# Optimization experiments

Hardware: AMD Instinct MI355X
Metric: run time of the kernel (lower is better)

Reference implementation:

```python
import jax, jax.numpy as jnp
import numpy as np

NUM_HEADS = 8
NUM_KV_HEADS = 2
HEAD_DIM = 256
HIDDEN = 2048
ROPE_THETA = 10000.0
QUERY_PRE_ATTN_SCALAR = 256.0
SOFTCAP = 50.0


def setup_inputs() -> dict:
    key = jax.random.key(0)
    k1, k2, k3, k4, k5 = jax.random.split(key, 5)
    B, S = 2, 2048
    s = 0.02
    return {
        "hidden_states": jax.random.normal(k1, (B, S, HIDDEN), dtype=jnp.float32),
        "Wq": jax.random.normal(k2, (NUM_HEADS * HEAD_DIM, HIDDEN), dtype=jnp.float32) * s,
        "Wk": jax.random.normal(k3, (NUM_KV_HEADS * HEAD_DIM, HIDDEN), dtype=jnp.float32) * s,
        "Wv": jax.random.normal(k4, (NUM_KV_HEADS * HEAD_DIM, HIDDEN), dtype=jnp.float32) * s,
        "Wo": jax.random.normal(k5, (HIDDEN, NUM_HEADS * HEAD_DIM), dtype=jnp.float32) * s,
    }


def _rope_cos_sin(S, dtype):
    # LlamaRotaryEmbedding: inv_freq over even dims, emb = cat(freqs, freqs)
    inv_freq = 1.0 / (ROPE_THETA ** (jnp.arange(0, HEAD_DIM, 2, dtype=jnp.float32) / HEAD_DIM))
    pos = jnp.arange(S, dtype=jnp.float32)
    freqs = pos[:, None] * inv_freq[None, :]          # [S, D/2]
    emb = jnp.concatenate([freqs, freqs], axis=-1)     # [S, D]
    return jnp.cos(emb).astype(dtype), jnp.sin(emb).astype(dtype)


def _rotate_half(x):
    x1, x2 = x[..., : HEAD_DIM // 2], x[..., HEAD_DIM // 2 :]
    return jnp.concatenate([-x2, x1], axis=-1)


def reference(hidden_states, Wq, Wk, Wv, Wo):
    B, S, _ = hidden_states.shape
    q = jnp.einsum('bsh,dh->bsd', hidden_states, Wq).reshape(B, S, NUM_HEADS, HEAD_DIM).transpose(0, 2, 1, 3)
    k = jnp.einsum('bsh,dh->bsd', hidden_states, Wk).reshape(B, S, NUM_KV_HEADS, HEAD_DIM).transpose(0, 2, 1, 3)
    v = jnp.einsum('bsh,dh->bsd', hidden_states, Wv).reshape(B, S, NUM_KV_HEADS, HEAD_DIM).transpose(0, 2, 1, 3)

    cos, sin = _rope_cos_sin(S, hidden_states.dtype)   # [S, D]
    cos = cos[None, None]                               # [1,1,S,D]
    sin = sin[None, None]
    q = q * cos + _rotate_half(q) * sin
    k = k * cos + _rotate_half(k) * sin

    # GQA expansion: repeat kv heads to match query heads
    groups = NUM_HEADS // NUM_KV_HEADS
    k = jnp.repeat(k, groups, axis=1)                   # [B,H,S,D]
    v = jnp.repeat(v, groups, axis=1)

    scale = QUERY_PRE_ATTN_SCALAR ** -0.5
    scores = jnp.einsum('bhqd,bhkd->bhqk', q, k) * scale
    scores = jnp.tanh(scores / SOFTCAP) * SOFTCAP       # logit softcapping
    probs = jax.nn.softmax(scores, axis=-1)             # NOTE: no causal mask in source
    attn = jnp.einsum('bhqk,bhkd->bhqd', probs, v)
    attn = attn.transpose(0, 2, 1, 3).reshape(B, S, NUM_HEADS * HEAD_DIM)
    return jnp.einsum('bsd,hd->bsh', attn, Wo)
```

## Files before the change

### kernel.cpp

```cpp
#include <hip/hip_runtime.h>
#include <hip/hip_bf16.h>

typedef __bf16 bf16;
typedef bf16 bf16x8 __attribute__((ext_vector_type(8)));
typedef bf16 bf16x4 __attribute__((ext_vector_type(4)));
typedef float f32x4 __attribute__((ext_vector_type(4)));

#define SEQ 2048
#define HID 2048

__device__ __forceinline__ void gload16(const bf16* gsrc, bf16* ldst) {
  __builtin_amdgcn_global_load_lds(
      (const __attribute__((address_space(1))) unsigned int*)gsrc,
      (__attribute__((address_space(3))) unsigned int*)ldst, 16, 0, 0);
}

__device__ __forceinline__ f32x4 mfma16(bf16x8 a, bf16x8 b, f32x4 c) {
  return __builtin_amdgcn_mfma_f32_16x16x32_bf16(a, b, c, 0, 0, 0);
}

__global__ void cast_bf16(const float* __restrict__ in, bf16* __restrict__ out, int n4) {
  int i = blockIdx.x * 256 + threadIdx.x;
  if (i >= n4) return;
  float4 v = ((const float4*)in)[i];
  bf16x4 o = { (bf16)v.x, (bf16)v.y, (bf16)v.z, (bf16)v.w };
  *(bf16x4*)(out + (size_t)i * 4) = o;
}

__global__ void rope_table(float2* __restrict__ tab) {
  int i = blockIdx.x * 256 + threadIdx.x;
  int s = i >> 7, dp = i & 127;
  float invf = powf(10000.0f, -(float)dp * (1.0f / 128.0f));
  float f = (float)s * invf;
  tab[i] = make_float2(cosf(f), sinf(f));
}

template <int H>
__global__ void rope_apply(bf16* __restrict__ X, const float2* __restrict__ tab) {
  int i = blockIdx.x * 256 + threadIdx.x;
  int dp = i & 127;
  int t = i >> 7;
  int h = t & (H - 1);
  int row = t / H;
  int s = row & (SEQ - 1);
  size_t base = (size_t)row * (H * 256) + h * 256;
  float2 cs = tab[s * 128 + dp];
  float x1 = (float)X[base + dp], x2 = (float)X[base + dp + 128];
  X[base + dp]       = (bf16)(x1 * cs.x - x2 * cs.y);
  X[base + dp + 128] = (bf16)(x2 * cs.x + x1 * cs.y);
}

template <int EPI>
__global__ void gemm_bt(const bf16* __restrict__ A, const bf16* __restrict__ B,
                        void* __restrict__ C, int M, int N, int K) {
  __shared__ __align__(16) bf16 la[128 * 64];
  __shared__ __align__(16) bf16 lb[128 * 64];
  const int tid = threadIdx.x;
  const int w = tid >> 6, l = tid & 63;
  const int lr = l & 15, lg = l >> 4;
  const int brow = blockIdx.x * 128, bcol = blockIdx.y * 128;
  const int wr = w >> 1, wc = w & 1;
  f32x4 acc[4][4];
  const f32x4 zero = {0.f, 0.f, 0.f, 0.f};
#pragma unroll
  for (int m = 0; m < 4; ++m)
#pragma unroll
    for (int n = 0; n < 4; ++n) acc[m][n] = zero;

  for (int k0 = 0; k0 < K; k0 += 64) {
#pragma unroll
    for (int p = 0; p < 4; ++p) {
      int gid = (p * 4 + w) * 64 + l;
      int row = gid >> 3, col = (gid & 7) * 8;
      gload16(&A[(size_t)(brow + row) * K + k0 + col], &la[(size_t)(p * 4 + w) * 512]);
      gload16(&B[(size_t)(bcol + row) * K + k0 + col], &lb[(size_t)(p * 4 + w) * 512]);
    }
    __syncthreads();
#pragma unroll
    for (int kk = 0; kk < 2; ++kk) {
      bf16x8 af[4], bfr[4];
#pragma unroll
      for (int m = 0; m < 4; ++m)
        af[m] = *(const bf16x8*)&la[(wr * 64 + m * 16 + lr) * 64 + kk * 32 + lg * 8];
#pragma unroll
      for (int n = 0; n < 4; ++n)
        bfr[n] = *(const bf16x8*)&lb[(wc * 64 + n * 16 + lr) * 64 + kk * 32 + lg * 8];
#pragma unroll
      for (int m = 0; m < 4; ++m)
#pragma unroll
        for (int n = 0; n < 4; ++n)
          acc[m][n] = mfma16(af[m], bfr[n], acc[m][n]);
    }
    __syncthreads();
  }

#pragma unroll
  for (int m = 0; m < 4; ++m) {
#pragma unroll
    for (int n = 0; n < 4; ++n) {
#pragma unroll
      for (int r = 0; r < 4; ++r) {
        int grow = brow + wr * 64 + m * 16 + lg * 4 + r;
        int gcol = bcol + wc * 64 + n * 16 + lr;
        float v = acc[m][n][r];
        if constexpr (EPI == 0) {
          ((bf16*)C)[(size_t)grow * N + gcol] = (bf16)v;
        } else if constexpr (EPI == 1) {
          int b = grow >> 11, s = grow & (SEQ - 1);
          int kv = gcol >> 8, d = gcol & 255;
          ((bf16*)C)[(((size_t)(b * 2 + kv)) * 256 + d) * SEQ + s] = (bf16)v;
        } else {
          ((float*)C)[(size_t)grow * N + gcol] = v;
        }
      }
    }
  }
}

__global__ __launch_bounds__(256, 2)
void attn(const bf16* __restrict__ Qp, const bf16* __restrict__ Kp,
          const bf16* __restrict__ Vt, bf16* __restrict__ Aout) {
  __shared__ __align__(16) bf16 Kl[64 * 256];
  __shared__ __align__(16) bf16 Vl[256 * 64];
  __shared__ __align__(16) bf16 Pl[64 * 64];
  const int tid = threadIdx.x, w = tid >> 6, l = tid & 63;
  const int lr = l & 15, lg = l >> 4;
  const int lin = blockIdx.x;
  const int work = (lin & 7) * 64 + (lin >> 3);
  const int bh = work >> 5;
  const int b = bh >> 3, h = bh & 7, kv = h >> 2;
  const int q0 = (work & 31) * 64;

  const bf16* qbase = Qp + ((size_t)(b * SEQ + q0 + w * 16 + lr)) * HID + h * 256;
  bf16x8 qf[8];
#pragma unroll
  for (int kc = 0; kc < 8; ++kc) qf[kc] = *(const bf16x8*)(qbase + kc * 32 + lg * 8);

  const f32x4 zero = {0.f, 0.f, 0.f, 0.f};
  f32x4 outa[16];
#pragma unroll
  for (int n = 0; n < 16; ++n) outa[n] = zero;
  float rs[4] = {0.f, 0.f, 0.f, 0.f};

  const bf16* kslab = Kp + (size_t)(b * SEQ) * 512 + kv * 256;
  const bf16* vslab = Vt + (size_t)((b * 2 + kv) * 256) * SEQ;

  for (int kt = 0; kt < 32; ++kt) {
    const int t0 = kt * 64;
#pragma unroll
    for (int p = 0; p < 8; ++p) {
      int gid = p * 256 + w * 64 + l;
      {
        int row = gid >> 5, g = gid & 31;
        gload16(kslab + (size_t)(t0 + row) * 512 + ((g ^ (row & 7)) * 8),
                &Kl[(p * 256 + w * 64) * 8]);
      }
      {
        int row = gid >> 3, g = gid & 7;
        gload16(vslab + (size_t)row * SEQ + t0 + ((g ^ (row & 7)) * 8),
                &Vl[(p * 256 + w * 64) * 8]);
      }
    }
    __syncthreads();

    f32x4 sc[4];
#pragma unroll
    for (int n = 0; n < 4; ++n) sc[n] = zero;
#pragma unroll
    for (int kc = 0; kc < 8; ++kc) {
#pragma unroll
      for (int n = 0; n < 4; ++n) {
        bf16x8 kf = *(const bf16x8*)&Kl[(n * 16 + lr) * 256 + (((kc * 4 + lg) ^ (lr & 7)) * 8)];
        sc[n] = mfma16(qf[kc], kf, sc[n]);
      }
    }

#pragma unroll
    for (int n = 0; n < 4; ++n) {
#pragma unroll
      for (int r = 0; r < 4; ++r) {
        float e1 = __expf(sc[n][r] * 0.0025f);
        float p = __expf(-100.0f * __builtin_amdgcn_rcpf(e1 + 1.0f));
        rs[r] += p;
        int prow = w * 16 + lg * 4 + r;
        int pcol = (n * 16 + lr) ^ ((prow & 7) << 3);
        Pl[prow * 64 + pcol] = (bf16)p;
      }
    }

#pragma unroll
    for (int kc2 = 0; kc2 < 2; ++kc2) {
      bf16x8 pf = *(const bf16x8*)&Pl[(w * 16 + lr) * 64 + (((kc2 * 4 + lg) ^ (lr & 7)) * 8)];
#pragma unroll
      for (int n = 0; n < 16; ++n) {
        bf16x8 vf = *(const bf16x8*)&Vl[(n * 16 + lr) * 64 + (((kc2 * 4 + lg) ^ (lr & 7)) * 8)];
        outa[n] = mfma16(pf, vf, outa[n]);
      }
    }
    __syncthreads();
  }

  float inv[4];
#pragma unroll
  for (int r = 0; r < 4; ++r) {
    float v = rs[r];
    v += __shfl_xor(v, 1, 16);
    v += __shfl_xor(v, 2, 16);
    v += __shfl_xor(v, 4, 16);
    v += __shfl_xor(v, 8, 16);
    inv[r] = 1.0f / v;
  }
  bf16* obase = Aout + ((size_t)(b * SEQ + q0 + w * 16 + lg * 4)) * HID + h * 256 + lr;
#pragma unroll
  for (int n = 0; n < 16; ++n)
#pragma unroll
    for (int r = 0; r < 4; ++r)
      obase[(size_t)r * HID + n * 16] = (bf16)(outa[n][r] * inv[r]);
}

extern "C" void kernel_launch(void* const* d_in, const int* in_sizes, int n_in,
                              void* d_out, int out_size, void* d_ws, size_t ws_size,
                              hipStream_t stream) {
  const float* hs = (const float*)d_in[0];
  const float* Wq = (const float*)d_in[1];
  const float* Wk = (const float*)d_in[2];
  const float* Wv = (const float*)d_in[3];
  const float* Wo = (const float*)d_in[4];
  float* out = (float*)d_out;
  char* ws = (char*)d_ws;

  bf16* hs_b  = (bf16*)(ws + 0);
  bf16* wq_b  = (bf16*)(ws + 16777216);
  bf16* wk_b  = (bf16*)(ws + 25165824);
  bf16* wv_b  = (bf16*)(ws + 27262976);
  bf16* wo_b  = (bf16*)(ws + 29360128);
  bf16* qp    = (bf16*)(ws + 37748736);
  bf16* kp    = (bf16*)(ws + 54525952);
  bf16* vt    = (bf16*)(ws + 58720256);
  float2* tab = (float2*)(ws + 62914560);
  bf16* aout  = hs_b;

  cast_bf16<<<8192, 256, 0, stream>>>(hs, hs_b, 2097152);
  cast_bf16<<<4096, 256, 0, stream>>>(Wq, wq_b, 1048576);
  cast_bf16<<<1024, 256, 0, stream>>>(Wk, wk_b, 262144);
  cast_bf16<<<1024, 256, 0, stream>>>(Wv, wv_b, 262144);
  cast_bf16<<<4096, 256, 0, stream>>>(Wo, wo_b, 1048576);
  rope_table<<<1024, 256, 0, stream>>>(tab);

  gemm_bt<0><<<dim3(32, 16), 256, 0, stream>>>(hs_b, wq_b, qp, 4096, 2048, 2048);
  gemm_bt<0><<<dim3(32, 4),  256, 0, stream>>>(hs_b, wk_b, kp, 4096, 512, 2048);
  gemm_bt<1><<<dim3(32, 4),  256, 0, stream>>>(hs_b, wv_b, vt, 4096, 512, 2048);

  rope_apply<8><<<16384, 256, 0, stream>>>(qp, tab);
  rope_apply<2><<<4096, 256, 0, stream>>>(kp, tab);

  attn<<<512, 256, 0, stream>>>(qp, kp, vt, aout);

  gemm_bt<2><<<dim3(32, 16), 256, 0, stream>>>(aout, wo_b, out, 4096, 2048, 2048);
}
```

Measured before the change: 415.9 us.

## Fuse QKV projections and double attention query tile with double-buffered K/V

The three Q/K/V projection GEMMs become one launch over a concatenated 3072-column weight. It relies on the bf16 weights sitting contiguously in the workspace, and it routes each output column range to its own destination and layout. The attention kernel now handles 128 queries per block, with two 16-row query tiles per wave, so each K/V tile loaded into LDS is reused twice. K/V staging is double-buffered, so the next tile's loads overlap the current compute. The cost is more LDS and registers, which cuts occupancy to one block per CU and halves the grid to 256 blocks.

```diff
diff --git a/kernel.cpp b/kernel.cpp
--- a/kernel.cpp
+++ b/kernel.cpp
@@ -52,7 +52,8 @@
 
 template <int EPI>
 __global__ void gemm_bt(const bf16* __restrict__ A, const bf16* __restrict__ B,
-                        void* __restrict__ C, int M, int N, int K) {
+                        void* __restrict__ C, void* __restrict__ C2,
+                        void* __restrict__ C3, int M, int N, int K) {
   __shared__ __align__(16) bf16 la[128 * 64];
   __shared__ __align__(16) bf16 lb[128 * 64];
   const int tid = threadIdx.x;
@@ -103,119 +104,147 @@
         int grow = brow + wr * 64 + m * 16 + lg * 4 + r;
         int gcol = bcol + wc * 64 + n * 16 + lr;
         float v = acc[m][n][r];
-        if constexpr (EPI == 0) {
-          ((bf16*)C)[(size_t)grow * N + gcol] = (bf16)v;
-        } else if constexpr (EPI == 1) {
-          int b = grow >> 11, s = grow & (SEQ - 1);
-          int kv = gcol >> 8, d = gcol & 255;
-          ((bf16*)C)[(((size_t)(b * 2 + kv)) * 256 + d) * SEQ + s] = (bf16)v;
+        if constexpr (EPI == 2) {
+          ((float*)C)[(size_t)grow * N + gcol] = v;
         } else {
-          ((float*)C)[(size_t)grow * N + gcol] = v;
+          if (gcol < 2048) {
+            ((bf16*)C)[(size_t)grow * 2048 + gcol] = (bf16)v;
+          } else if (gcol < 2560) {
+            ((bf16*)C2)[(size_t)grow * 512 + (gcol - 2048)] = (bf16)v;
+          } else {
+            int kvcol = gcol - 2560;
+            int b = grow >> 11, s = grow & (SEQ - 1);
+            int kv = kvcol >> 8, d = kvcol & 255;
+            ((bf16*)C3)[(((size_t)(b * 2 + kv)) * 256 + d) * SEQ + s] = (bf16)v;
+          }
         }
       }
     }
   }
 }
 
-__global__ __launch_bounds__(256, 2)
+__global__ __launch_bounds__(256, 1)
 void attn(const bf16* __restrict__ Qp, const bf16* __restrict__ Kp,
           const bf16* __restrict__ Vt, bf16* __restrict__ Aout) {
-  __shared__ __align__(16) bf16 Kl[64 * 256];
-  __shared__ __align__(16) bf16 Vl[256 * 64];
-  __shared__ __align__(16) bf16 Pl[64 * 64];
+  __shared__ __align__(16) bf16 Kl[2][64 * 256];
+  __shared__ __align__(16) bf16 Vl[2][256 * 64];
+  __shared__ __align__(16) bf16 Pl[128 * 64];
   const int tid = threadIdx.x, w = tid >> 6, l = tid & 63;
   const int lr = l & 15, lg = l >> 4;
   const int lin = blockIdx.x;
-  const int work = (lin & 7) * 64 + (lin >> 3);
-  const int bh = work >> 5;
+  const int work = (lin & 7) * 32 + (lin >> 3);
+  const int bh = work >> 4;
   const int b = bh >> 3, h = bh & 7, kv = h >> 2;
-  const int q0 = (work & 31) * 64;
-
-  const bf16* qbase = Qp + ((size_t)(b * SEQ + q0 + w * 16 + lr)) * HID + h * 256;
-  bf16x8 qf[8];
-#pragma unroll
-  for (int kc = 0; kc < 8; ++kc) qf[kc] = *(const bf16x8*)(qbase + kc * 32 + lg * 8);
+  const int q0 = (work & 15) * 128;
+
+  bf16x8 qf[2][8];
+#pragma unroll
+  for (int m = 0; m < 2; ++m) {
+    const bf16* qb = Qp + ((size_t)(b * SEQ + q0 + w * 32 + m * 16 + lr)) * HID + h * 256;
+#pragma unroll
+    for (int kc = 0; kc < 8; ++kc) qf[m][kc] = *(const bf16x8*)(qb + kc * 32 + lg * 8);
+  }
 
   const f32x4 zero = {0.f, 0.f, 0.f, 0.f};
-  f32x4 outa[16];
-#pragma unroll
-  for (int n = 0; n < 16; ++n) outa[n] = zero;
-  float rs[4] = {0.f, 0.f, 0.f, 0.f};
+  f32x4 outa[2][16];
+#pragma unroll
+  for (int m = 0; m < 2; ++m)
+#pragma unroll
+    for (int n = 0; n < 16; ++n) outa[m][n] = zero;
+  float rs[2][4] = {{0.f, 0.f, 0.f, 0.f}, {0.f, 0.f, 0.f, 0.f}};
 
   const bf16* kslab = Kp + (size_t)(b * SEQ) * 512 + kv * 256;
   const bf16* vslab = Vt + (size_t)((b * 2 + kv) * 256) * SEQ;
 
-  for (int kt = 0; kt < 32; ++kt) {
-    const int t0 = kt * 64;
+  auto stage = [&](int buf, int ktile) {
+    const int t0s = ktile * 64;
 #pragma unroll
     for (int p = 0; p < 8; ++p) {
-      int gid = p * 256 + w * 64 + l;
+      int gid = p * 256 + tid;
       {
         int row = gid >> 5, g = gid & 31;
-        gload16(kslab + (size_t)(t0 + row) * 512 + ((g ^ (row & 7)) * 8),
-                &Kl[(p * 256 + w * 64) * 8]);
+        gload16(kslab + (size_t)(t0s + row) * 512 + ((g ^ (row & 7)) * 8),
+                &Kl[buf][(p * 256 + w * 64) * 8]);
       }
       {
         int row = gid >> 3, g = gid & 7;
-        gload16(vslab + (size_t)row * SEQ + t0 + ((g ^ (row & 7)) * 8),
-                &Vl[(p * 256 + w * 64) * 8]);
+        gload16(vslab + (size_t)row * SEQ + t0s + ((g ^ (row & 7)) * 8),
+                &Vl[buf][(p * 256 + w * 64) * 8]);
+      }
+    }
+  };
+
+  stage(0, 0);
+  __syncthreads();
+
+  for (int kt = 0; kt < 32; ++kt) {
+    const int cur = kt & 1;
+    if (kt < 31) stage(cur ^ 1, kt + 1);
+
+    f32x4 sc[2][4];
+#pragma unroll
+    for (int m = 0; m < 2; ++m)
+#pragma unroll
+      for (int n = 0; n < 4; ++n) sc[m][n] = zero;
+#pragma unroll
+    for (int kc = 0; kc < 8; ++kc) {
+#pragma unroll
+      for (int n = 0; n < 4; ++n) {
+        bf16x8 kf = *(const bf16x8*)&Kl[cur][(n * 16 + lr) * 256 + (((kc * 4 + lg) ^ (lr & 7)) * 8)];
+        sc[0][n] = mfma16(qf[0][kc], kf, sc[0][n]);
+        sc[1][n] = mfma16(qf[1][kc], kf, sc[1][n]);
+      }
+    }
+
+#pragma unroll
+    for (int m = 0; m < 2; ++m) {
+#pragma unroll
+      for (int n = 0; n < 4; ++n) {
+#pragma unroll
+        for (int r = 0; r < 4; ++r) {
+          float e1 = __expf(sc[m][n][r] * 0.0025f);
+          float p = __expf(-100.0f * __builtin_amdgcn_rcpf(e1 + 1.0f));
+          rs[m][r] += p;
+          int prow = w * 32 + m * 16 + lg * 4 + r;
+          int pcol = (n * 16 + lr) ^ ((prow & 7) << 3);
+          Pl[prow * 64 + pcol] = (bf16)p;
+        }
+      }
+    }
+
+#pragma unroll
+    for (int kc2 = 0; kc2 < 2; ++kc2) {
+      bf16x8 pf0 = *(const bf16x8*)&Pl[(w * 32 + lr) * 64 + (((kc2 * 4 + lg) ^ (lr & 7)) * 8)];
+      bf16x8 pf1 = *(const bf16x8*)&Pl[(w * 32 + 16 + lr) * 64 + (((kc2 * 4 + lg) ^ (lr & 7)) * 8)];
+#pragma unroll
+      for (int n = 0; n < 16; ++n) {
+        bf16x8 vf = *(const bf16x8*)&Vl[cur][(n * 16 + lr) * 64 + (((kc2 * 4 + lg) ^ (lr & 7)) * 8)];
+        outa[0][n] = mfma16(pf0, vf, outa[0][n]);
+        outa[1][n] = mfma16(pf1, vf, outa[1][n]);
       }
     }
     __syncthreads();
-
-    f32x4 sc[4];
-#pragma unroll
-    for (int n = 0; n < 4; ++n) sc[n] = zero;
-#pragma unroll
-    for (int kc = 0; kc < 8; ++kc) {
-#pragma unroll
-      for (int n = 0; n < 4; ++n) {
-        bf16x8 kf = *(const bf16x8*)&Kl[(n * 16 + lr) * 256 + (((kc * 4 + lg) ^ (lr & 7)) * 8)];
-        sc[n] = mfma16(qf[kc], kf, sc[n]);
-      }
-    }
-
-#pragma unroll
-    for (int n = 0; n < 4; ++n) {
-#pragma unroll
-      for (int r = 0; r < 4; ++r) {
-        float e1 = __expf(sc[n][r] * 0.0025f);
-        float p = __expf(-100.0f * __builtin_amdgcn_rcpf(e1 + 1.0f));
-        rs[r] += p;
-        int prow = w * 16 + lg * 4 + r;
-        int pcol = (n * 16 + lr) ^ ((prow & 7) << 3);
-        Pl[prow * 64 + pcol] = (bf16)p;
-      }
-    }
-
-#pragma unroll
-    for (int kc2 = 0; kc2 < 2; ++kc2) {
-      bf16x8 pf = *(const bf16x8*)&Pl[(w * 16 + lr) * 64 + (((kc2 * 4 + lg) ^ (lr & 7)) * 8)];
-#pragma unroll
-      for (int n = 0; n < 16; ++n) {
-        bf16x8 vf = *(const bf16x8*)&Vl[(n * 16 + lr) * 64 + (((kc2 * 4 + lg) ^ (lr & 7)) * 8)];
-        outa[n] = mfma16(pf, vf, outa[n]);
-      }
-    }
-    __syncthreads();
-  }
-
-  float inv[4];
-#pragma unroll
-  for (int r = 0; r < 4; ++r) {
-    float v = rs[r];
-    v += __shfl_xor(v, 1, 16);
-    v += __shfl_xor(v, 2, 16);
-    v += __shfl_xor(v, 4, 16);
-    v += __shfl_xor(v, 8, 16);
-    inv[r] = 1.0f / v;
-  }
-  bf16* obase = Aout + ((size_t)(b * SEQ + q0 + w * 16 + lg * 4)) * HID + h * 256 + lr;
-#pragma unroll
-  for (int n = 0; n < 16; ++n)
-#pragma unroll
-    for (int r = 0; r < 4; ++r)
-      obase[(size_t)r * HID + n * 16] = (bf16)(outa[n][r] * inv[r]);
+  }
+
+#pragma unroll
+  for (int m = 0; m < 2; ++m) {
+    float inv[4];
+#pragma unroll
+    for (int r = 0; r < 4; ++r) {
+      float v = rs[m][r];
+      v += __shfl_xor(v, 1, 16);
+      v += __shfl_xor(v, 2, 16);
+      v += __shfl_xor(v, 4, 16);
+      v += __shfl_xor(v, 8, 16);
+      inv[r] = 1.0f / v;
+    }
+    bf16* ob = Aout + ((size_t)(b * SEQ + q0 + w * 32 + m * 16 + lg * 4)) * HID + h * 256 + lr;
+#pragma unroll
+    for (int n = 0; n < 16; ++n)
+#pragma unroll
+      for (int r = 0; r < 4; ++r)
+        ob[(size_t)r * HID + n * 16] = (bf16)(outa[m][n][r] * inv[r]);
+  }
 }
 
 extern "C" void kernel_launch(void* const* d_in, const int* in_sizes, int n_in,
@@ -247,14 +276,12 @@
   cast_bf16<<<4096, 256, 0, stream>>>(Wo, wo_b, 1048576);
   rope_table<<<1024, 256, 0, stream>>>(tab);
 
-  gemm_bt<0><<<dim3(32, 16), 256, 0, stream>>>(hs_b, wq_b, qp, 4096, 2048, 2048);
-  gemm_bt<0><<<dim3(32, 4),  256, 0, stream>>>(hs_b, wk_b, kp, 4096, 512, 2048);
-  gemm_bt<1><<<dim3(32, 4),  256, 0, stream>>>(hs_b, wv_b, vt, 4096, 512, 2048);
+  gemm_bt<3><<<dim3(32, 24), 256, 0, stream>>>(hs_b, wq_b, qp, kp, vt, 4096, 3072, 2048);
 
   rope_apply<8><<<16384, 256, 0, stream>>>(qp, tab);
   rope_apply<2><<<4096, 256, 0, stream>>>(kp, tab);
 
-  attn<<<512, 256, 0, stream>>>(qp, kp, vt, aout);
-
-  gemm_bt<2><<<dim3(32, 16), 256, 0, stream>>>(aout, wo_b, out, 4096, 2048, 2048);
-}
+  attn<<<256, 256, 0, stream>>>(qp, kp, vt, aout);
+
+  gemm_bt<2><<<dim3(32, 16), 256, 0, stream>>>(aout, wo_b, out, nullptr, nullptr, 4096, 2048, 2048);
+}
```

New measurement: 395.4 us. -4.9%, faster.

## Fuse QKV projections into one GEMM and transpose score MFMA for vector P stores

Applied to the files above, without the earlier changes.

Replaces three separate Q, K, V projection GEMM launches with a single GEMM over a concatenated weight (wq_b, wk_b, wv_b laid out contiguously in the workspace), routing output columns to the Q, K, or transposed-V buffers in the epilogue. In attention, the score MFMA operands are swapped so each lane holds four consecutive keys for one query row. This allows 4-wide bf16 stores into the P tile and a single per-lane row-sum reduced with two cross-lane shuffles. The fusion relies on the weight buffers being adjacent in memory and adds branching to the GEMM epilogue.

```diff
diff --git a/kernel.cpp b/kernel.cpp
--- a/kernel.cpp
+++ b/kernel.cpp
@@ -52,7 +52,8 @@
 
 template <int EPI>
 __global__ void gemm_bt(const bf16* __restrict__ A, const bf16* __restrict__ B,
-                        void* __restrict__ C, int M, int N, int K) {
+                        void* __restrict__ C, void* __restrict__ C2,
+                        void* __restrict__ C3, int M, int N, int K) {
   __shared__ __align__(16) bf16 la[128 * 64];
   __shared__ __align__(16) bf16 lb[128 * 64];
   const int tid = threadIdx.x;
@@ -103,14 +104,19 @@
         int grow = brow + wr * 64 + m * 16 + lg * 4 + r;
         int gcol = bcol + wc * 64 + n * 16 + lr;
         float v = acc[m][n][r];
-        if constexpr (EPI == 0) {
-          ((bf16*)C)[(size_t)grow * N + gcol] = (bf16)v;
-        } else if constexpr (EPI == 1) {
-          int b = grow >> 11, s = grow & (SEQ - 1);
-          int kv = gcol >> 8, d = gcol & 255;
-          ((bf16*)C)[(((size_t)(b * 2 + kv)) * 256 + d) * SEQ + s] = (bf16)v;
+        if constexpr (EPI == 2) {
+          ((float*)C)[(size_t)grow * N + gcol] = v;
         } else {
-          ((float*)C)[(size_t)grow * N + gcol] = v;
+          if (gcol < 2048) {
+            ((bf16*)C)[(size_t)grow * 2048 + gcol] = (bf16)v;
+          } else if (gcol < 2560) {
+            ((bf16*)C2)[(size_t)grow * 512 + (gcol - 2048)] = (bf16)v;
+          } else {
+            int kvcol = gcol - 2560;
+            int b = grow >> 11, s = grow & (SEQ - 1);
+            int kv = kvcol >> 8, d = kvcol & 255;
+            ((bf16*)C3)[(((size_t)(b * 2 + kv)) * 256 + d) * SEQ + s] = (bf16)v;
+          }
         }
       }
     }
@@ -140,7 +146,7 @@
   f32x4 outa[16];
 #pragma unroll
   for (int n = 0; n < 16; ++n) outa[n] = zero;
-  float rs[4] = {0.f, 0.f, 0.f, 0.f};
+  float rs = 0.f;
 
   const bf16* kslab = Kp + (size_t)(b * SEQ) * 512 + kv * 256;
   const bf16* vslab = Vt + (size_t)((b * 2 + kv) * 256) * SEQ;
@@ -171,21 +177,23 @@
 #pragma unroll
       for (int n = 0; n < 4; ++n) {
         bf16x8 kf = *(const bf16x8*)&Kl[(n * 16 + lr) * 256 + (((kc * 4 + lg) ^ (lr & 7)) * 8)];
-        sc[n] = mfma16(qf[kc], kf, sc[n]);
+        sc[n] = mfma16(kf, qf[kc], sc[n]);
       }
     }
 
 #pragma unroll
     for (int n = 0; n < 4; ++n) {
+      bf16x4 pv;
 #pragma unroll
       for (int r = 0; r < 4; ++r) {
         float e1 = __expf(sc[n][r] * 0.0025f);
         float p = __expf(-100.0f * __builtin_amdgcn_rcpf(e1 + 1.0f));
-        rs[r] += p;
-        int prow = w * 16 + lg * 4 + r;
-        int pcol = (n * 16 + lr) ^ ((prow & 7) << 3);
-        Pl[prow * 64 + pcol] = (bf16)p;
-      }
+        rs += p;
+        pv[r] = (bf16)p;
+      }
+      int prow = w * 16 + lr;
+      int g = (n * 2 + (lg >> 1)) ^ (lr & 7);
+      *(bf16x4*)&Pl[prow * 64 + g * 8 + (lg & 1) * 4] = pv;
     }
 
 #pragma unroll
@@ -200,22 +208,19 @@
     __syncthreads();
   }
 
-  float inv[4];
-#pragma unroll
-  for (int r = 0; r < 4; ++r) {
-    float v = rs[r];
-    v += __shfl_xor(v, 1, 16);
-    v += __shfl_xor(v, 2, 16);
-    v += __shfl_xor(v, 4, 16);
-    v += __shfl_xor(v, 8, 16);
-    inv[r] = 1.0f / v;
-  }
+  rs += __shfl_xor(rs, 16);
+  rs += __shfl_xor(rs, 32);
+  float inv = 1.0f / rs;
+  float invr[4];
+#pragma unroll
+  for (int r = 0; r < 4; ++r) invr[r] = __shfl(inv, lg * 4 + r, 16);
+
   bf16* obase = Aout + ((size_t)(b * SEQ + q0 + w * 16 + lg * 4)) * HID + h * 256 + lr;
 #pragma unroll
   for (int n = 0; n < 16; ++n)
 #pragma unroll
     for (int r = 0; r < 4; ++r)
-      obase[(size_t)r * HID + n * 16] = (bf16)(outa[n][r] * inv[r]);
+      obase[(size_t)r * HID + n * 16] = (bf16)(outa[n][r] * invr[r]);
 }
 
 extern "C" void kernel_launch(void* const* d_in, const int* in_sizes, int n_in,
@@ -247,14 +252,12 @@
   cast_bf16<<<4096, 256, 0, stream>>>(Wo, wo_b, 1048576);
   rope_table<<<1024, 256, 0, stream>>>(tab);
 
-  gemm_bt<0><<<dim3(32, 16), 256, 0, stream>>>(hs_b, wq_b, qp, 4096, 2048, 2048);
-  gemm_bt<0><<<dim3(32, 4),  256, 0, stream>>>(hs_b, wk_b, kp, 4096, 512, 2048);
-  gemm_bt<1><<<dim3(32, 4),  256, 0, stream>>>(hs_b, wv_b, vt, 4096, 512, 2048);
+  gemm_bt<3><<<dim3(32, 24), 256, 0, stream>>>(hs_b, wq_b, qp, kp, vt, 4096, 3072, 2048);
 
   rope_apply<8><<<16384, 256, 0, stream>>>(qp, tab);
   rope_apply<2><<<4096, 256, 0, stream>>>(kp, tab);
 
   attn<<<512, 256, 0, stream>>>(qp, kp, vt, aout);
 
-  gemm_bt<2><<<dim3(32, 16), 256, 0, stream>>>(aout, wo_b, out, 4096, 2048, 2048);
-}
+  gemm_bt<2><<<dim3(32, 16), 256, 0, stream>>>(aout, wo_b, out, nullptr, nullptr, 4096, 2048, 2048);
+}
```

After: 340.5 us. 1.22x faster.
